# Optimization experiments

Measured on AMD Instinct MI355X. Metric: run time of the kernel, lower is better.

## Reference

```python
import jax, jax.numpy as jnp
import numpy as np

CONNECTION_STRENGTH = 3.0   # hardcoded in AMN.forward
DIRECT_WEIGHT = 1.5         # direct_weight_initial
CONN_THRESHOLD = 0.1


def setup_inputs() -> dict:
    key = jax.random.key(0)
    k1, k2, k3, k4, k5 = jax.random.split(key, 5)
    U, T, N = 128, 256, 1024
    return {
        "input_spikes": (jax.random.uniform(k1, (T, N)) < 0.1).astype(jnp.float32),
        "unit_outputs": jax.random.uniform(k2, (U, T, N), dtype=jnp.float32),  # stacked ModularUnit outputs
        "conn": jax.random.uniform(k3, (U, U), dtype=jnp.float32),             # sampled connection matrix
        "target_spikes": (jax.random.uniform(k4, (T, N)) < 0.3).astype(jnp.float32),  # encode_number output
        "rand_bias": jax.random.uniform(k5, (T, N), dtype=jnp.float32),        # torch.rand_like for boost
    }


def reference(input_spikes, unit_outputs, conn, target_spikes, rand_bias):
    # get_spike_rate: mean firing rate in Hz (spikes.mean() * 1000)
    input_rate = input_spikes.mean() * 1000.0
    target_rate = input_rate + 20.0

    # Fused threshold-gated weighted aggregation:
    # for i,j: if conn[i,j] > 0.1: final += unit_outputs[j] * conn[i,j] * 3.0
    gated = jnp.where(conn > CONN_THRESHOLD, conn, 0.0)           # [U,U]
    w = CONNECTION_STRENGTH * gated.sum(axis=0)                   # [U] total inbound weight per source j
    final = jnp.einsum('j,jtn->tn', w, unit_outputs)              # [T,N]

    # Direct mapping heuristic
    final = final * 0.5 + target_spikes * DIRECT_WEIGHT

    # Conditional boost when mean activity is low
    mean = final.mean()
    target_mean = target_rate / 100.0
    boost = jnp.maximum(0.0, target_mean - mean)
    final = jnp.where(mean < 0.2, final + rand_bias * boost * 2.0, final)
    return final
```

## Files before the change

kernel.cpp:

```cpp
#include <hip/hip_runtime.h>

#define U    128
#define TN   (256 * 1024)
#define TN4  (TN / 4)
#define NBLK 256

typedef float vfloat4 __attribute__((ext_vector_type(4)));


__global__ __launch_bounds__(256) void fused_kernel(const float*   __restrict__ conn,
                                                    const vfloat4* __restrict__ uo,
                                                    const vfloat4* __restrict__ tgt,
                                                    const vfloat4* __restrict__ insp,
                                                    vfloat4*       __restrict__ out,
                                                    float*         __restrict__ ws) {
    __shared__ float wpart[2][U];
    __shared__ float w_s[U];
    __shared__ float red[8];
    int tid = threadIdx.x;
    int idx = blockIdx.x * 256 + tid;

    vfloat4 t  = tgt[idx];
    vfloat4 is = insp[idx];

    {
        int j = tid & 127;
        int h = tid >> 7;
        const float* cp = conn + (size_t)(h * 64) * U + j;
        float s = 0.0f;
#pragma unroll
        for (int k = 0; k < 64; ++k) {
            float v = cp[(size_t)k * U];
            s += (v > 0.1f) ? v : 0.0f;
        }
        wpart[h][j] = s;
    }
    __syncthreads();
    if (tid < U) w_s[tid] = 3.0f * (wpart[0][tid] + wpart[1][tid]);
    __syncthreads();

    const vfloat4* p = uo + idx;
    vfloat4 acc = 0.0f;
#pragma unroll 16
    for (int jj = 0; jj < U; ++jj)
        acc += w_s[jj] * __builtin_nontemporal_load(p + (size_t)jj * TN4);

    vfloat4 r = acc * 0.5f + 1.5f * t;
    __builtin_nontemporal_store(r, out + idx);

    float lsum = r.x + r.y + r.z + r.w;
    float lin  = is.x + is.y + is.z + is.w;
#pragma unroll
    for (int off = 32; off > 0; off >>= 1) {
        lsum += __shfl_down(lsum, off, 64);
        lin  += __shfl_down(lin,  off, 64);
    }
    int wave = tid >> 6;
    int lane = tid & 63;
    if (lane == 0) { red[wave] = lsum; red[4 + wave] = lin; }
    __syncthreads();
    if (tid == 0) {
        ws[blockIdx.x]        = red[0] + red[1] + red[2] + red[3];
        ws[NBLK + blockIdx.x] = red[4] + red[5] + red[6] + red[7];
    }
}

__global__ __launch_bounds__(256) void boost_kernel(const vfloat4* __restrict__ rb,
                                                    vfloat4*       __restrict__ out,
                                                    const float*   __restrict__ ws) {
    int tid = threadIdx.x;
    float lsum = ws[tid];
    float lin  = ws[NBLK + tid];
#pragma unroll
    for (int off = 32; off > 0; off >>= 1) {
        lsum += __shfl_down(lsum, off, 64);
        lin  += __shfl_down(lin,  off, 64);
    }
    __shared__ float red[8];
    int wave = tid >> 6;
    int lane = tid & 63;
    if (lane == 0) { red[wave] = lsum; red[4 + wave] = lin; }
    __syncthreads();
    float tot = red[0] + red[1] + red[2] + red[3];
    float tin = red[4] + red[5] + red[6] + red[7];

    float mean        = tot * (1.0f / TN);
    float in_rate     = tin * (1000.0f / TN);
    float target_mean = (in_rate + 20.0f) * 0.01f;
    float boost       = fmaxf(0.0f, target_mean - mean);
    if (mean < 0.2f) {
        int idx = blockIdx.x * 256 + tid;
        out[idx] += rb[idx] * (boost * 2.0f);
    }
}

extern "C" void kernel_launch(void* const* d_in, const int* in_sizes, int n_in,
                              void* d_out, int out_size, void* d_ws, size_t ws_size,
                              hipStream_t stream) {
    const float* input_spikes = (const float*)d_in[0];
    const float* unit_outputs = (const float*)d_in[1];
    const float* conn         = (const float*)d_in[2];
    const float* target       = (const float*)d_in[3];
    const float* rand_bias    = (const float*)d_in[4];
    float* out = (float*)d_out;
    float* ws  = (float*)d_ws;

    fused_kernel<<<NBLK, 256, 0, stream>>>(
        conn, (const vfloat4*)unit_outputs, (const vfloat4*)target,
        (const vfloat4*)input_spikes, (vfloat4*)out, ws);

    boost_kernel<<<TN4 / 256, 256, 0, stream>>>(
        (const vfloat4*)rand_bias, (vfloat4*)out, ws);
}
```

Before: 190.4 us.

## Fuse boost pass into main kernel via last-block ticket and prefetch unit loads

Removes the separate boost kernel. The last block to finish, detected with an atomic ticket, does the global reduction and applies the conditional boost serially over the whole output. The first 16 unit_output loads are issued before the connection-matrix reduction to overlap their latency, and the 0.5 scale is folded into the weights. This adds a memset launch and an atomic, and if the boost branch is taken, one block must stream the whole output alone.

```diff
diff --git a/kernel.cpp b/kernel.cpp
--- a/kernel.cpp
+++ b/kernel.cpp
@@ -4,24 +4,34 @@
 #define TN   (256 * 1024)
 #define TN4  (TN / 4)
 #define NBLK 256
+#define PF   16
 
 typedef float vfloat4 __attribute__((ext_vector_type(4)));
 
 
-__global__ __launch_bounds__(256) void fused_kernel(const float*   __restrict__ conn,
-                                                    const vfloat4* __restrict__ uo,
-                                                    const vfloat4* __restrict__ tgt,
-                                                    const vfloat4* __restrict__ insp,
-                                                    vfloat4*       __restrict__ out,
-                                                    float*         __restrict__ ws) {
+__global__ __launch_bounds__(256, 1) void fused_kernel(const float*   __restrict__ conn,
+                                                       const vfloat4* __restrict__ uo,
+                                                       const vfloat4* __restrict__ tgt,
+                                                       const vfloat4* __restrict__ insp,
+                                                       const vfloat4* __restrict__ rb,
+                                                       vfloat4*       __restrict__ out,
+                                                       float*         __restrict__ ws,
+                                                       unsigned int*  __restrict__ ticket) {
     __shared__ float wpart[2][U];
     __shared__ float w_s[U];
     __shared__ float red[8];
+    __shared__ int   is_last_s;
     int tid = threadIdx.x;
     int idx = blockIdx.x * 256 + tid;
 
     vfloat4 t  = tgt[idx];
     vfloat4 is = insp[idx];
+
+    const vfloat4* p = uo + idx;
+    vfloat4 pre[PF];
+#pragma unroll
+    for (int k = 0; k < PF; ++k)
+        pre[k] = __builtin_nontemporal_load(p + (size_t)k * TN4);
 
     {
         int j = tid & 127;
@@ -36,16 +46,18 @@
         wpart[h][j] = s;
     }
     __syncthreads();
-    if (tid < U) w_s[tid] = 3.0f * (wpart[0][tid] + wpart[1][tid]);
+    if (tid < U) w_s[tid] = 1.5f * (wpart[0][tid] + wpart[1][tid]);
     __syncthreads();
 
-    const vfloat4* p = uo + idx;
     vfloat4 acc = 0.0f;
+#pragma unroll
+    for (int k = 0; k < PF; ++k)
+        acc += w_s[k] * pre[k];
 #pragma unroll 16
-    for (int jj = 0; jj < U; ++jj)
+    for (int jj = PF; jj < U; ++jj)
         acc += w_s[jj] * __builtin_nontemporal_load(p + (size_t)jj * TN4);
 
-    vfloat4 r = acc * 0.5f + 1.5f * t;
+    vfloat4 r = acc + 1.5f * t;
     __builtin_nontemporal_store(r, out + idx);
 
     float lsum = r.x + r.y + r.z + r.w;
@@ -62,24 +74,22 @@
     if (tid == 0) {
         ws[blockIdx.x]        = red[0] + red[1] + red[2] + red[3];
         ws[NBLK + blockIdx.x] = red[4] + red[5] + red[6] + red[7];
+        __threadfence();
+        unsigned int prev = atomicAdd(ticket, 1u);
+        is_last_s = (prev == NBLK - 1);
     }
-}
+    __syncthreads();
+    if (!is_last_s) return;
 
-__global__ __launch_bounds__(256) void boost_kernel(const vfloat4* __restrict__ rb,
-                                                    vfloat4*       __restrict__ out,
-                                                    const float*   __restrict__ ws) {
-    int tid = threadIdx.x;
-    float lsum = ws[tid];
-    float lin  = ws[NBLK + tid];
+    __threadfence();
+    float a = ws[tid];
+    float b = ws[NBLK + tid];
 #pragma unroll
     for (int off = 32; off > 0; off >>= 1) {
-        lsum += __shfl_down(lsum, off, 64);
-        lin  += __shfl_down(lin,  off, 64);
+        a += __shfl_down(a, off, 64);
+        b += __shfl_down(b, off, 64);
     }
-    __shared__ float red[8];
-    int wave = tid >> 6;
-    int lane = tid & 63;
-    if (lane == 0) { red[wave] = lsum; red[4 + wave] = lin; }
+    if (lane == 0) { red[wave] = a; red[4 + wave] = b; }
     __syncthreads();
     float tot = red[0] + red[1] + red[2] + red[3];
     float tin = red[4] + red[5] + red[6] + red[7];
@@ -89,8 +99,11 @@
     float target_mean = (in_rate + 20.0f) * 0.01f;
     float boost       = fmaxf(0.0f, target_mean - mean);
     if (mean < 0.2f) {
-        int idx = blockIdx.x * 256 + tid;
-        out[idx] += rb[idx] * (boost * 2.0f);
+        float s2 = boost * 2.0f;
+        for (int i = tid; i < TN4; i += 256) {
+            vfloat4 o = out[i];
+            out[i] = o + rb[i] * s2;
+        }
     }
 }
 
@@ -105,10 +118,11 @@
     float* out = (float*)d_out;
     float* ws  = (float*)d_ws;
 
+    unsigned int* ticket = (unsigned int*)(ws + 2 * NBLK);
+    hipMemsetAsync(ticket, 0, sizeof(unsigned int), stream);
+
     fused_kernel<<<NBLK, 256, 0, stream>>>(
         conn, (const vfloat4*)unit_outputs, (const vfloat4*)target,
-        (const vfloat4*)input_spikes, (vfloat4*)out, ws);
-
-    boost_kernel<<<TN4 / 256, 256, 0, stream>>>(
-        (const vfloat4*)rand_bias, (vfloat4*)out, ws);
+        (const vfloat4*)input_spikes, (const vfloat4*)rand_bias,
+        (vfloat4*)out, ws, ticket);
 }
```

Measured after the change: 202.3 us. 1.06x slower.
